# Kernel optimization log

Measured on AMD Instinct MI355X. Metric: run time of the kernel, lower is better.

The kernel has to match this reference:

```python
import jax, jax.numpy as jnp
import numpy as np

B, N, D = 4, 4096, 1024
H, DH = 16, 64
EPS = 1e-5


def setup_inputs() -> dict:
    key = jax.random.key(0)
    ks = jax.random.split(key, 4)
    x = jax.random.normal(ks[0], (B, N, D), dtype=jnp.float32)
    w_qkv = jax.random.normal(ks[1], (D, 3 * H * DH), dtype=jnp.float32) * 0.02
    # per-head LayerNorm affine params (one LayerNorm(dim_head) per head)
    gamma_k = jnp.ones((H, DH), dtype=jnp.float32)
    beta_k = jnp.zeros((H, DH), dtype=jnp.float32)
    gamma_v = jnp.ones((H, DH), dtype=jnp.float32)
    beta_v = jnp.zeros((H, DH), dtype=jnp.float32)
    w_out = jax.random.normal(ks[2], (H * DH, D), dtype=jnp.float32) * 0.02
    b_out = jnp.zeros((D,), dtype=jnp.float32)
    return {"x": x, "w_qkv": w_qkv, "gamma_k": gamma_k, "beta_k": beta_k,
            "gamma_v": gamma_v, "beta_v": beta_v, "w_out": w_out, "b_out": b_out}


def _per_head_layernorm(t, gamma, beta):
    # t: [b, h, n, d]; gamma/beta: [h, d] (distinct affine per head)
    mu = jnp.mean(t, axis=-1, keepdims=True)
    var = jnp.mean(jnp.square(t - mu), axis=-1, keepdims=True)  # biased, as torch LayerNorm
    tn = (t - mu) * jax.lax.rsqrt(var + EPS)
    return tn * gamma[None, :, None, :] + beta[None, :, None, :]


def reference(x, w_qkv, gamma_k, beta_k, gamma_v, beta_v, w_out, b_out):
    b, n, _ = x.shape
    h, dh = gamma_k.shape
    qkv = jnp.einsum('bnd,de->bne', x, w_qkv)  # [b, n, 3*h*dh]
    q, k, v = jnp.split(qkv, 3, axis=-1)

    def to_heads(t):  # b n (h d) -> b h n d
        return t.reshape(b, n, h, dh).transpose(0, 2, 1, 3)

    q, k, v = to_heads(q), to_heads(k), to_heads(v)
    k = _per_head_layernorm(k, gamma_k, beta_k)
    v = _per_head_layernorm(v, gamma_v, beta_v)
    # linear attention: scores = k^T v / n  -> [b, h, d, d]
    scores = jnp.einsum('bhnd,bhne->bhde', k, v) / n
    out = jnp.einsum('bhnd,bhde->bhne', q, scores)  # [b, h, n, d]
    out = out.transpose(0, 2, 1, 3).reshape(b, n, h * dh)
    return jnp.einsum('bne,ed->bnd', out, w_out) + b_out
```

## Files before the change

### kernel.cpp

```cpp
#include <hip/hip_runtime.h>

typedef __attribute__((ext_vector_type(4))) float f32x4;
typedef __attribute__((ext_vector_type(8))) short s16x8;

#define DEV static __device__ __forceinline__

typedef __attribute__((address_space(3))) void lds_t;
typedef __attribute__((address_space(1))) void gbl_t;

DEV void gload_lds16(const void* g, void* l) {
    __builtin_amdgcn_global_load_lds((gbl_t*)g, (lds_t*)l, 16, 0, 0);
}

DEV ushort f2bf(float f) {
    unsigned u = __float_as_uint(f);
    u += 0x7fffu + ((u >> 16) & 1u);
    return (ushort)(u >> 16);
}
DEV float bf2f(ushort h) { return __uint_as_float(((unsigned)h) << 16); }

#define FULLBAR() do {                              \
    __builtin_amdgcn_sched_barrier(0);              \
    asm volatile("" ::: "memory");                  \
    __builtin_amdgcn_s_barrier();                   \
    asm volatile("" ::: "memory");                  \
    __builtin_amdgcn_sched_barrier(0);              \
} while (0)

#define WAITVM(n) asm volatile("s_waitcnt vmcnt(" #n ")" ::: "memory")

__global__ void pack_x_k(const float* __restrict__ x, ushort* __restrict__ xb, int n4) {
    int stride = gridDim.x * blockDim.x;
    for (int i = blockIdx.x * blockDim.x + threadIdx.x; i < n4; i += stride) {
        float4 v = reinterpret_cast<const float4*>(x)[i];
        ushort4 o;
        o.x = f2bf(v.x); o.y = f2bf(v.y); o.z = f2bf(v.z); o.w = f2bf(v.w);
        reinterpret_cast<ushort4*>(xb)[i] = o;
    }
}

__global__ void pack_wq_k(const float* __restrict__ w, ushort* __restrict__ o) {
    int i = blockIdx.x * 256 + threadIdx.x;
    int r = i >> 8, c4 = i & 255;
    float4 v = *reinterpret_cast<const float4*>(w + (size_t)r * 3072 + c4 * 4);
    ushort4 u;
    u.x = f2bf(v.x); u.y = f2bf(v.y); u.z = f2bf(v.z); u.w = f2bf(v.w);
    *reinterpret_cast<ushort4*>(o + (size_t)r * 1024 + c4 * 4) = u;
}

__global__ void trans_pack_k(const float* __restrict__ in, ushort* __restrict__ out,
                             int R, int C, int col0) {
    __shared__ float tile[32][33];
    int bx = col0 + blockIdx.x * 32, by = blockIdx.y * 32;
    int tx = threadIdx.x, ty = threadIdx.y;
#pragma unroll
    for (int i = 0; i < 32; i += 8)
        tile[ty + i][tx] = in[(size_t)(by + ty + i) * C + bx + tx];
    __syncthreads();
#pragma unroll
    for (int i = 0; i < 32; i += 8)
        out[(size_t)(bx - col0 + ty + i) * R + by + tx] = f2bf(tile[tx][ty + i]);
}

template <int MODE>
__global__ __launch_bounds__(512, 2) void gemm_bt_k(
    const ushort* __restrict__ A, const ushort* __restrict__ Bt,
    int Nn, int col0, size_t b_stride,
    ushort* __restrict__ qo, ushort* __restrict__ ko, ushort* __restrict__ vo,
    const float* __restrict__ gk, const float* __restrict__ bk,
    const float* __restrict__ gv, const float* __restrict__ bv,
    const float* __restrict__ bias, float* __restrict__ outf)
{
    __shared__ __align__(16) ushort SH[65536];
    const int t = threadIdx.x;
    const int w = t >> 6, lane = t & 63;
    const int wr = w >> 2, wc = w & 3;
    const int lrow = lane & 15, kh = lane >> 4;

    int bid = blockIdx.y * gridDim.x + blockIdx.x;
    int C8 = (gridDim.x * gridDim.y) >> 3;
    int nid = (bid & 7) * C8 + (bid >> 3);
    int n0 = (nid % gridDim.x) * 256;
    int m0 = (nid / gridDim.x) * 256;

    const ushort* Bte = (MODE == 1) ? Bt + (size_t)(m0 >> 12) * b_stride : Bt;

    const int srow = w * 8 + (lane >> 3);
    const int scol = ((lane & 7) ^ ((lane >> 3) & 7)) * 8;

    f32x4 acc[8][4] = {};

    auto STAGE = [&](int kt, int s) {
        ushort* As = SH + s * 32768;
        ushort* Bs = As + 16384;
        const ushort* Ag = A   + (size_t)(m0 + srow) * 1024 + kt * 64 + scol;
        const ushort* Bg = Bte + (size_t)(n0 + srow) * 1024 + kt * 64 + scol;
#pragma unroll
        for (int c = 0; c < 4; ++c) {
            gload_lds16(Ag + (size_t)(c * 64) * 1024, As + (c * 64 + w * 8) * 64);
            gload_lds16(Bg + (size_t)(c * 64) * 1024, Bs + (c * 64 + w * 8) * 64);
        }
    };

    const int g0 = ((kh) ^ (lrow & 7)) * 8;
    const int g1 = ((4 + kh) ^ (lrow & 7)) * 8;

    auto COMPUTE = [&](int s) {
        const ushort* As = SH + s * 32768;
        const ushort* Bs = As + 16384;
#pragma unroll
        for (int kk = 0; kk < 2; ++kk) {
            const int go = kk ? g1 : g0;
            s16x8 af[8], bfr[4];
#pragma unroll
            for (int mi = 0; mi < 8; mi++)
                af[mi] = *reinterpret_cast<const s16x8*>(&As[(wr * 128 + mi * 16 + lrow) * 64 + go]);
#pragma unroll
            for (int ni = 0; ni < 4; ni++)
                bfr[ni] = *reinterpret_cast<const s16x8*>(&Bs[(wc * 64 + ni * 16 + lrow) * 64 + go]);
            __builtin_amdgcn_s_setprio(1);
#pragma unroll
            for (int mi = 0; mi < 8; mi++)
#pragma unroll
                for (int ni = 0; ni < 4; ni++)
                    acc[mi][ni] = __builtin_amdgcn_mfma_f32_16x16x32_bf16(af[mi], bfr[ni], acc[mi][ni], 0, 0, 0);
            __builtin_amdgcn_s_setprio(0);
        }
    };

    STAGE(0, 0);
    for (int kt = 0; kt < 15; ++kt) {
        STAGE(kt + 1, (kt + 1) & 1);
        WAITVM(8);
        FULLBAR();
        COMPUTE(kt & 1);
        FULLBAR();
    }
    WAITVM(0);
    FULLBAR();
    COMPUTE(1);

    if (MODE == 0) {
        const int e0 = col0 + n0 + wc * 64;
        const int which = e0 >> 10;
        const int h = (e0 >> 6) & 15;
        const float* g  = (which == 1) ? gk : gv;
        const float* bb = (which == 1) ? bk : bv;
        ushort* dst     = (which == 1) ? ko : vo;
        float gr[4], br[4];
#pragma unroll
        for (int ni = 0; ni < 4; ni++) {
            gr[ni] = g[h * 64 + ni * 16 + lrow];
            br[ni] = bb[h * 64 + ni * 16 + lrow];
        }
        __syncthreads();
        ushort* Tl = SH + w * 4608;
#pragma unroll
        for (int chunk = 0; chunk < 2; ++chunk) {
#pragma unroll
            for (int mi2 = 0; mi2 < 4; ++mi2) {
                const int mi = chunk * 4 + mi2;
#pragma unroll
                for (int j = 0; j < 4; j++) {
                    float s = acc[mi][0][j] + acc[mi][1][j] + acc[mi][2][j] + acc[mi][3][j];
                    s += __shfl_xor(s, 1, 64);
                    s += __shfl_xor(s, 2, 64);
                    s += __shfl_xor(s, 4, 64);
                    s += __shfl_xor(s, 8, 64);
                    float mu = s * (1.f / 64.f);
                    float t2 = 0.f;
#pragma unroll
                    for (int ni = 0; ni < 4; ni++) {
                        float dd = acc[mi][ni][j] - mu;
                        t2 += dd * dd;
                    }
                    t2 += __shfl_xor(t2, 1, 64);
                    t2 += __shfl_xor(t2, 2, 64);
                    t2 += __shfl_xor(t2, 4, 64);
                    t2 += __shfl_xor(t2, 8, 64);
                    float inv = rsqrtf(t2 * (1.f / 64.f) + 1e-5f);
#pragma unroll
                    for (int ni = 0; ni < 4; ni++) {
                        float y = (acc[mi][ni][j] - mu) * inv * gr[ni] + br[ni];
                        Tl[(ni * 16 + lrow) * 72 + mi2 * 16 + kh * 4 + j] = f2bf(y);
                    }
                }
            }
            const int mrow0 = m0 + wr * 128 + chunk * 64;
            const int b = mrow0 >> 12, ns0 = mrow0 & 4095;
            ushort* obase = dst + (((size_t)b * 16 + h) * 64) * 4096 + ns0;
#pragma unroll
            for (int p = 0; p < 8; ++p) {
                int d = p * 8 + (lane >> 3);
                int mo = (lane & 7) * 8;
                s16x8 vv = *reinterpret_cast<const s16x8*>(&Tl[d * 72 + mo]);
                *reinterpret_cast<s16x8*>(obase + (size_t)d * 4096 + mo) = vv;
            }
        }
    } else if (MODE == 1) {
#pragma unroll
        for (int mi = 0; mi < 8; mi++)
#pragma unroll
            for (int ni = 0; ni < 4; ni++) {
                int e = n0 + wc * 64 + ni * 16 + lrow;
                float bv2 = bias[e];
#pragma unroll
                for (int j = 0; j < 4; j++) {
                    int m = m0 + wr * 128 + mi * 16 + kh * 4 + j;
                    outf[(size_t)m * Nn + e] = acc[mi][ni][j] + bv2;
                }
            }
    } else {
#pragma unroll
        for (int mi = 0; mi < 8; mi++)
#pragma unroll
            for (int ni = 0; ni < 4; ni++) {
                int e = n0 + wc * 64 + ni * 16 + lrow;
#pragma unroll
                for (int j = 0; j < 4; j++) {
                    int m = m0 + wr * 128 + mi * 16 + kh * 4 + j;
                    qo[(size_t)m * 1024 + e] = f2bf(acc[mi][ni][j]);
                }
            }
    }
}

__global__ __launch_bounds__(256) void scores_k(const ushort* __restrict__ kT,
                                                const ushort* __restrict__ vT,
                                                float* __restrict__ sc)
{
    __shared__ float red[4][64][65];
    const int bh = blockIdx.y;
    const int t = threadIdx.x;
    const int w = t >> 6, lane = t & 63;
    const int lrow = lane & 15, kh = lane >> 4;
    const ushort* ka = kT + (size_t)bh * 64 * 4096;
    const ushort* va = vT + (size_t)bh * 64 * 4096;
    const int n0 = blockIdx.x * 512 + w * 128;

    f32x4 acc[4][4] = {};
#pragma unroll
    for (int ks = 0; ks < 4; ++ks) {
        const int n = n0 + ks * 32 + kh * 8;
        s16x8 af[4], bfr[4];
#pragma unroll
        for (int mi = 0; mi < 4; mi++)
            af[mi] = *reinterpret_cast<const s16x8*>(ka + (size_t)(mi * 16 + lrow) * 4096 + n);
#pragma unroll
        for (int ni = 0; ni < 4; ni++)
            bfr[ni] = *reinterpret_cast<const s16x8*>(va + (size_t)(ni * 16 + lrow) * 4096 + n);
#pragma unroll
        for (int mi = 0; mi < 4; mi++)
#pragma unroll
            for (int ni = 0; ni < 4; ni++)
                acc[mi][ni] = __builtin_amdgcn_mfma_f32_16x16x32_bf16(af[mi], bfr[ni], acc[mi][ni], 0, 0, 0);
    }
#pragma unroll
    for (int mi = 0; mi < 4; mi++)
#pragma unroll
        for (int ni = 0; ni < 4; ni++)
#pragma unroll
            for (int j = 0; j < 4; j++)
                red[w][mi * 16 + kh * 4 + j][ni * 16 + lrow] = acc[mi][ni][j];
    __syncthreads();
    const float scale = 1.f / 4096.f;
    for (int idx = t; idx < 4096; idx += 256) {
        int d = idx >> 6, e = idx & 63;
        float s = red[0][d][e] + red[1][d][e] + red[2][d][e] + red[3][d][e];
        atomicAdd(&sc[(size_t)bh * 4096 + idx], s * scale);
    }
}

__global__ __launch_bounds__(256) void wprime_k(const float* __restrict__ sc,
                                                const ushort* __restrict__ woutT,
                                                ushort* __restrict__ wpT)
{
    __shared__ float scl[64][65];
    __shared__ ushort wl[128][72];
    int bh = blockIdx.y;
    int b = bh >> 4, h = bh & 15;
    int f0 = blockIdx.x * 128;
    int t = threadIdx.x;
    for (int i = t; i < 4096; i += 256) {
        int d2 = i >> 6, e = i & 63;
        scl[e][d2] = sc[(size_t)bh * 4096 + i];
    }
    for (int i = t; i < 1024; i += 256) {
        int fl = i >> 3, c = i & 7;
        *reinterpret_cast<int4*>(&wl[fl][c * 8]) =
            *reinterpret_cast<const int4*>(woutT + (size_t)(f0 + fl) * 1024 + h * 64 + c * 8);
    }
    __syncthreads();
    int dd = (t & 7) * 8;
    int fl0 = t >> 3;
#pragma unroll
    for (int fi = 0; fi < 4; ++fi) {
        int fl = fi * 32 + fl0;
        float acc[8] = {};
        for (int e = 0; e < 64; ++e) {
            float wv = bf2f(wl[fl][e]);
#pragma unroll
            for (int i = 0; i < 8; ++i)
                acc[i] = fmaf(wv, scl[e][dd + i], acc[i]);
        }
        ushort4 o0, o1;
        o0.x = f2bf(acc[0]); o0.y = f2bf(acc[1]); o0.z = f2bf(acc[2]); o0.w = f2bf(acc[3]);
        o1.x = f2bf(acc[4]); o1.y = f2bf(acc[5]); o1.z = f2bf(acc[6]); o1.w = f2bf(acc[7]);
        ushort* op = wpT + ((size_t)b * 1024 + f0 + fl) * 1024 + h * 64 + dd;
        *reinterpret_cast<ushort4*>(op) = o0;
        *reinterpret_cast<ushort4*>(op + 4) = o1;
    }
}

extern "C" void kernel_launch(void* const* d_in, const int* in_sizes, int n_in,
                              void* d_out, int out_size, void* d_ws, size_t ws_size,
                              hipStream_t stream)
{
    const float* x       = (const float*)d_in[0];
    const float* w_qkv   = (const float*)d_in[1];
    const float* gamma_k = (const float*)d_in[2];
    const float* beta_k  = (const float*)d_in[3];
    const float* gamma_v = (const float*)d_in[4];
    const float* beta_v  = (const float*)d_in[5];
    const float* w_out   = (const float*)d_in[6];
    const float* b_out   = (const float*)d_in[7];
    float* out = (float*)d_out;

    char* ws = (char*)d_ws;
    const size_t MB = 1024 * 1024;
    ushort* xb    = (ushort*)(ws);
    ushort* wkvT  = (ushort*)(ws + 32 * MB);
    ushort* woutT = (ushort*)(ws + 38 * MB);
    ushort* wqb   = (ushort*)(ws + 40 * MB);
    ushort* kb    = (ushort*)(ws + 48 * MB);
    ushort* vb    = (ushort*)(ws + 80 * MB);
    float*  sc    = (float*)(ws + 112 * MB);
    ushort* wpT   = (ushort*)(ws + 120 * MB);
    ushort* fT    = (ushort*)(ws + 128 * MB);

    pack_x_k<<<2048, 256, 0, stream>>>(x, xb, 16384 * 1024 / 4);
    pack_wq_k<<<1024, 256, 0, stream>>>(w_qkv, wqb);
    trans_pack_k<<<dim3(64, 32), dim3(32, 8), 0, stream>>>(w_qkv, wkvT, 1024, 3072, 1024);
    trans_pack_k<<<dim3(32, 32), dim3(32, 8), 0, stream>>>(w_out, woutT, 1024, 1024, 0);
    gemm_bt_k<0><<<dim3(8, 64), 512, 0, stream>>>(xb, wkvT, 2048, 1024, 0,
                                                  nullptr, kb, vb,
                                                  gamma_k, beta_k, gamma_v, beta_v,
                                                  nullptr, nullptr);
    hipMemsetAsync(sc, 0, 64 * 4096 * sizeof(float), stream);
    scores_k<<<dim3(8, 64), 256, 0, stream>>>(kb, vb, sc);
    wprime_k<<<dim3(8, 64), 256, 0, stream>>>(sc, woutT, wpT);
    gemm_bt_k<2><<<dim3(4, 16), 512, 0, stream>>>(wpT, wqb, 1024, 0, 0,
                                                  fT, nullptr, nullptr,
                                                  nullptr, nullptr, nullptr, nullptr,
                                                  nullptr, nullptr);
    gemm_bt_k<1><<<dim3(4, 64), 512, 0, stream>>>(xb, fT, 1024, 0, (size_t)1048576,
                                                  nullptr, nullptr, nullptr,
                                                  nullptr, nullptr, nullptr, nullptr,
                                                  b_out, out);
}
```

Measured before the change: 225.6 us.

## Split GEMM main loop into four interleaved sub-phases with staggered A/B prefetch

Restructures the bf16 MFMA GEMM main loop so each K tile is processed in four sub-phases of two M-fragments each. Global-to-LDS loads for the next A tile and the tile after next for B are issued between phases, and B fragments are loaded once per tile and held in registers. The aim is to overlap LDS reads, global loads and MFMA work more finely, in the style of a ping-pong schedule. It adds many more barriers per tile and depends on the vmcnt accounting staying correct.

```diff
diff --git a/kernel.cpp b/kernel.cpp
--- a/kernel.cpp
+++ b/kernel.cpp
@@ -28,6 +28,10 @@
 } while (0)
 
 #define WAITVM(n) asm volatile("s_waitcnt vmcnt(" #n ")" ::: "memory")
+#define LGKM0() do {                                        \
+    asm volatile("s_waitcnt lgkmcnt(0)" ::: "memory");      \
+    __builtin_amdgcn_sched_barrier(0);                      \
+} while (0)
 
 __global__ void pack_x_k(const float* __restrict__ x, ushort* __restrict__ xb, int n4) {
     int stride = gridDim.x * blockDim.x;
@@ -85,60 +89,92 @@
 
     const ushort* Bte = (MODE == 1) ? Bt + (size_t)(m0 >> 12) * b_stride : Bt;
 
-    const int srow = w * 8 + (lane >> 3);
+    const int srow8 = w * 8 + (lane >> 3);
     const int scol = ((lane & 7) ^ ((lane >> 3) & 7)) * 8;
 
+    const int g0 = ((kh) ^ (lrow & 7)) * 8;
+    const int g1 = ((4 + kh) ^ (lrow & 7)) * 8;
+
     f32x4 acc[8][4] = {};
-
-    auto STAGE = [&](int kt, int s) {
+    s16x8 bfr[4][2];
+
+    auto STAGE_A = [&](int kt, int s, int h) {
         ushort* As = SH + s * 32768;
-        ushort* Bs = As + 16384;
-        const ushort* Ag = A   + (size_t)(m0 + srow) * 1024 + kt * 64 + scol;
-        const ushort* Bg = Bte + (size_t)(n0 + srow) * 1024 + kt * 64 + scol;
-#pragma unroll
-        for (int c = 0; c < 4; ++c) {
-            gload_lds16(Ag + (size_t)(c * 64) * 1024, As + (c * 64 + w * 8) * 64);
-            gload_lds16(Bg + (size_t)(c * 64) * 1024, Bs + (c * 64 + w * 8) * 64);
+        const ushort* Ag = A + (size_t)(m0 + h * 128 + srow8) * 1024 + kt * 64 + scol;
+        gload_lds16(Ag,                     As + (h * 128 + w * 8) * 64);
+        gload_lds16(Ag + (size_t)64 * 1024, As + (h * 128 + 64 + w * 8) * 64);
+    };
+    auto STAGE_B = [&](int kt, int s, int h) {
+        ushort* Bs = SH + s * 32768 + 16384;
+        const ushort* Bg = Bte + (size_t)(n0 + h * 128 + srow8) * 1024 + kt * 64 + scol;
+        gload_lds16(Bg,                     Bs + (h * 128 + w * 8) * 64);
+        gload_lds16(Bg + (size_t)64 * 1024, Bs + (h * 128 + 64 + w * 8) * 64);
+    };
+    auto DS_B = [&](int s) {
+        const ushort* Bs = SH + s * 32768 + 16384;
+#pragma unroll
+        for (int ni = 0; ni < 4; ni++) {
+            const int r = (wc * 64 + ni * 16 + lrow) * 64;
+            bfr[ni][0] = *reinterpret_cast<const s16x8*>(&Bs[r + g0]);
+            bfr[ni][1] = *reinterpret_cast<const s16x8*>(&Bs[r + g1]);
         }
     };
 
-    const int g0 = ((kh) ^ (lrow & 7)) * 8;
-    const int g1 = ((4 + kh) ^ (lrow & 7)) * 8;
-
-    auto COMPUTE = [&](int s) {
-        const ushort* As = SH + s * 32768;
-        const ushort* Bs = As + 16384;
-#pragma unroll
-        for (int kk = 0; kk < 2; ++kk) {
-            const int go = kk ? g1 : g0;
-            s16x8 af[8], bfr[4];
-#pragma unroll
-            for (int mi = 0; mi < 8; mi++)
-                af[mi] = *reinterpret_cast<const s16x8*>(&As[(wr * 128 + mi * 16 + lrow) * 64 + go]);
-#pragma unroll
-            for (int ni = 0; ni < 4; ni++)
-                bfr[ni] = *reinterpret_cast<const s16x8*>(&Bs[(wc * 64 + ni * 16 + lrow) * 64 + go]);
-            __builtin_amdgcn_s_setprio(1);
-#pragma unroll
-            for (int mi = 0; mi < 8; mi++)
-#pragma unroll
-                for (int ni = 0; ni < 4; ni++)
-                    acc[mi][ni] = __builtin_amdgcn_mfma_f32_16x16x32_bf16(af[mi], bfr[ni], acc[mi][ni], 0, 0, 0);
-            __builtin_amdgcn_s_setprio(0);
-        }
-    };
-
-    STAGE(0, 0);
-    for (int kt = 0; kt < 15; ++kt) {
-        STAGE(kt + 1, (kt + 1) & 1);
-        WAITVM(8);
+#define DSA(MI0)                                                              \
+    _Pragma("unroll")                                                         \
+    for (int i = 0; i < 2; i++) {                                             \
+        const int r = (wr * 128 + ((MI0) + i) * 16 + lrow) * 64;              \
+        af[i][0] = *reinterpret_cast<const s16x8*>(&As[r + g0]);              \
+        af[i][1] = *reinterpret_cast<const s16x8*>(&As[r + g1]);              \
+    }
+
+#define MFMA16(MI0)                                                           \
+    __builtin_amdgcn_s_setprio(1);                                            \
+    _Pragma("unroll")                                                         \
+    for (int kk = 0; kk < 2; kk++)                                            \
+        _Pragma("unroll")                                                     \
+        for (int i = 0; i < 2; i++)                                           \
+            _Pragma("unroll")                                                 \
+            for (int ni = 0; ni < 4; ni++)                                    \
+                acc[(MI0) + i][ni] = __builtin_amdgcn_mfma_f32_16x16x32_bf16( \
+                    af[i][kk], bfr[ni][kk], acc[(MI0) + i][ni], 0, 0, 0);     \
+    __builtin_amdgcn_s_setprio(0);
+
+    STAGE_A(0, 0, 0); STAGE_A(0, 0, 1);
+    STAGE_B(0, 0, 0); STAGE_B(0, 0, 1);
+    STAGE_B(1, 1, 0); STAGE_B(1, 1, 1);
+    WAITVM(4);
+    FULLBAR();
+
+    for (int kt = 0; kt < 16; ++kt) {
+        const int p = kt & 1, q = p ^ 1;
+        const ushort* As = SH + p * 32768;
+        s16x8 af[2][2];
+        DS_B(p);
+        DSA(0);
+        if (kt + 1 < 16) STAGE_A(kt + 1, q, 0);
+        FULLBAR(); LGKM0();
+        MFMA16(0);
         FULLBAR();
-        COMPUTE(kt & 1);
+        DSA(2);
+        if (kt + 1 < 16) STAGE_A(kt + 1, q, 1);
+        FULLBAR(); LGKM0();
+        MFMA16(2);
         FULLBAR();
-    }
-    WAITVM(0);
-    FULLBAR();
-    COMPUTE(1);
+        DSA(4);
+        if (kt + 2 < 16) STAGE_B(kt + 2, p, 0);
+        FULLBAR(); LGKM0();
+        MFMA16(4);
+        FULLBAR();
+        DSA(6);
+        if (kt + 2 < 16) STAGE_B(kt + 2, p, 1);
+        if (kt < 14) { WAITVM(4); } else { WAITVM(0); }
+        FULLBAR(); LGKM0();
+        MFMA16(6);
+        FULLBAR();
+    }
+#undef DSA
+#undef MFMA16
 
     if (MODE == 0) {
         const int e0 = col0 + n0 + wc * 64;
@@ -190,8 +226,8 @@
             const int b = mrow0 >> 12, ns0 = mrow0 & 4095;
             ushort* obase = dst + (((size_t)b * 16 + h) * 64) * 4096 + ns0;
 #pragma unroll
-            for (int p = 0; p < 8; ++p) {
-                int d = p * 8 + (lane >> 3);
+            for (int p2 = 0; p2 < 8; ++p2) {
+                int d = p2 * 8 + (lane >> 3);
                 int mo = (lane & 7) * 8;
                 s16x8 vv = *reinterpret_cast<const s16x8*>(&Tl[d * 72 + mo]);
                 *reinterpret_cast<s16x8*>(obase + (size_t)d * 4096 + mo) = vv;
```

New measurement: 223.8 us. About the same (-0.8%).

## Restage GEMM pipeline with split A/B prefetch and add dedicated fold GEMM kernel

Applied to the files above, without the earlier changes.

The main bf16 GEMM loop is restructured: B tiles are prefetched two k-steps ahead and A tiles one step ahead, and each k-step is split into two half-k MFMA phases. Loads are issued between the phases, so the second barrier per iteration sits in the middle of the compute instead of at the end. Launch bounds change from 2 to 1 blocks per CU, allowing more registers per thread, since B fragments for both halves are now held. The small weight-folding GEMM (MODE 2, a 4x16 grid of 256x256 tiles) is replaced by a separate 128x128-tile kernel with a 3-stage pipeline, launched as 256 blocks to fill more CUs.

```diff
diff --git a/kernel.cpp b/kernel.cpp
--- a/kernel.cpp
+++ b/kernel.cpp
@@ -28,6 +28,7 @@
 } while (0)
 
 #define WAITVM(n) asm volatile("s_waitcnt vmcnt(" #n ")" ::: "memory")
+#define LGKM0() asm volatile("s_waitcnt lgkmcnt(0)" ::: "memory")
 
 __global__ void pack_x_k(const float* __restrict__ x, ushort* __restrict__ xb, int n4) {
     int stride = gridDim.x * blockDim.x;
@@ -63,10 +64,10 @@
 }
 
 template <int MODE>
-__global__ __launch_bounds__(512, 2) void gemm_bt_k(
+__global__ __launch_bounds__(512, 1) void gemm_bt_k(
     const ushort* __restrict__ A, const ushort* __restrict__ Bt,
     int Nn, int col0, size_t b_stride,
-    ushort* __restrict__ qo, ushort* __restrict__ ko, ushort* __restrict__ vo,
+    ushort* __restrict__ ko, ushort* __restrict__ vo,
     const float* __restrict__ gk, const float* __restrict__ bk,
     const float* __restrict__ gv, const float* __restrict__ bv,
     const float* __restrict__ bias, float* __restrict__ outf)
@@ -85,60 +86,76 @@
 
     const ushort* Bte = (MODE == 1) ? Bt + (size_t)(m0 >> 12) * b_stride : Bt;
 
-    const int srow = w * 8 + (lane >> 3);
+    const int srow8 = w * 8 + (lane >> 3);
     const int scol = ((lane & 7) ^ ((lane >> 3) & 7)) * 8;
-
-    f32x4 acc[8][4] = {};
-
-    auto STAGE = [&](int kt, int s) {
-        ushort* As = SH + s * 32768;
-        ushort* Bs = As + 16384;
-        const ushort* Ag = A   + (size_t)(m0 + srow) * 1024 + kt * 64 + scol;
-        const ushort* Bg = Bte + (size_t)(n0 + srow) * 1024 + kt * 64 + scol;
-#pragma unroll
-        for (int c = 0; c < 4; ++c) {
-            gload_lds16(Ag + (size_t)(c * 64) * 1024, As + (c * 64 + w * 8) * 64);
-            gload_lds16(Bg + (size_t)(c * 64) * 1024, Bs + (c * 64 + w * 8) * 64);
-        }
-    };
 
     const int g0 = ((kh) ^ (lrow & 7)) * 8;
     const int g1 = ((4 + kh) ^ (lrow & 7)) * 8;
 
-    auto COMPUTE = [&](int s) {
-        const ushort* As = SH + s * 32768;
+    f32x4 acc[8][4] = {};
+    s16x8 bfr[4][2];
+    s16x8 af[8];
+
+    auto STAGE_A = [&](int kt, int s, int h) {
+        ushort* As = SH + s * 32768;
+        const ushort* Ag = A + (size_t)(m0 + h * 128 + srow8) * 1024 + kt * 64 + scol;
+        gload_lds16(Ag,                     As + (h * 128 + w * 8) * 64);
+        gload_lds16(Ag + (size_t)64 * 1024, As + (h * 128 + 64 + w * 8) * 64);
+    };
+    auto STAGE_B = [&](int kt, int s, int h) {
+        ushort* Bs = SH + s * 32768 + 16384;
+        const ushort* Bg = Bte + (size_t)(n0 + h * 128 + srow8) * 1024 + kt * 64 + scol;
+        gload_lds16(Bg,                     Bs + (h * 128 + w * 8) * 64);
+        gload_lds16(Bg + (size_t)64 * 1024, Bs + (h * 128 + 64 + w * 8) * 64);
+    };
+
+    STAGE_A(0, 0, 0); STAGE_A(0, 0, 1);
+    STAGE_B(0, 0, 0); STAGE_B(0, 0, 1);
+    STAGE_B(1, 1, 0); STAGE_B(1, 1, 1);
+
+    for (int kt = 0; kt < 16; ++kt) {
+        const int p = kt & 1, q = p ^ 1;
+        const ushort* As = SH + p * 32768;
         const ushort* Bs = As + 16384;
-#pragma unroll
-        for (int kk = 0; kk < 2; ++kk) {
-            const int go = kk ? g1 : g0;
-            s16x8 af[8], bfr[4];
-#pragma unroll
-            for (int mi = 0; mi < 8; mi++)
-                af[mi] = *reinterpret_cast<const s16x8*>(&As[(wr * 128 + mi * 16 + lrow) * 64 + go]);
+
+        if (kt < 15) { WAITVM(4); } else { WAITVM(0); }
+        FULLBAR();
+
+#pragma unroll
+        for (int ni = 0; ni < 4; ni++) {
+            const int r = (wc * 64 + ni * 16 + lrow) * 64;
+            bfr[ni][0] = *reinterpret_cast<const s16x8*>(&Bs[r + g0]);
+            bfr[ni][1] = *reinterpret_cast<const s16x8*>(&Bs[r + g1]);
+        }
+#pragma unroll
+        for (int mi = 0; mi < 8; mi++)
+            af[mi] = *reinterpret_cast<const s16x8*>(&As[(wr * 128 + mi * 16 + lrow) * 64 + g0]);
+        if (kt + 1 < 16) { STAGE_A(kt + 1, q, 0); STAGE_A(kt + 1, q, 1); }
+
+        __builtin_amdgcn_s_setprio(1);
+#pragma unroll
+        for (int mi = 0; mi < 8; mi++)
 #pragma unroll
             for (int ni = 0; ni < 4; ni++)
-                bfr[ni] = *reinterpret_cast<const s16x8*>(&Bs[(wc * 64 + ni * 16 + lrow) * 64 + go]);
-            __builtin_amdgcn_s_setprio(1);
-#pragma unroll
-            for (int mi = 0; mi < 8; mi++)
-#pragma unroll
-                for (int ni = 0; ni < 4; ni++)
-                    acc[mi][ni] = __builtin_amdgcn_mfma_f32_16x16x32_bf16(af[mi], bfr[ni], acc[mi][ni], 0, 0, 0);
-            __builtin_amdgcn_s_setprio(0);
-        }
-    };
-
-    STAGE(0, 0);
-    for (int kt = 0; kt < 15; ++kt) {
-        STAGE(kt + 1, (kt + 1) & 1);
-        WAITVM(8);
+                acc[mi][ni] = __builtin_amdgcn_mfma_f32_16x16x32_bf16(af[mi], bfr[ni][0], acc[mi][ni], 0, 0, 0);
+        __builtin_amdgcn_s_setprio(0);
+
+        LGKM0();
         FULLBAR();
-        COMPUTE(kt & 1);
-        FULLBAR();
-    }
-    WAITVM(0);
-    FULLBAR();
-    COMPUTE(1);
+
+        if (kt + 2 < 16) { STAGE_B(kt + 2, p, 0); STAGE_B(kt + 2, p, 1); }
+#pragma unroll
+        for (int mi = 0; mi < 8; mi++)
+            af[mi] = *reinterpret_cast<const s16x8*>(&As[(wr * 128 + mi * 16 + lrow) * 64 + g1]);
+
+        __builtin_amdgcn_s_setprio(1);
+#pragma unroll
+        for (int mi = 0; mi < 8; mi++)
+#pragma unroll
+            for (int ni = 0; ni < 4; ni++)
+                acc[mi][ni] = __builtin_amdgcn_mfma_f32_16x16x32_bf16(af[mi], bfr[ni][1], acc[mi][ni], 0, 0, 0);
+        __builtin_amdgcn_s_setprio(0);
+    }
 
     if (MODE == 0) {
         const int e0 = col0 + n0 + wc * 64;
@@ -190,14 +207,14 @@
             const int b = mrow0 >> 12, ns0 = mrow0 & 4095;
             ushort* obase = dst + (((size_t)b * 16 + h) * 64) * 4096 + ns0;
 #pragma unroll
-            for (int p = 0; p < 8; ++p) {
-                int d = p * 8 + (lane >> 3);
+            for (int p2 = 0; p2 < 8; ++p2) {
+                int d = p2 * 8 + (lane >> 3);
                 int mo = (lane & 7) * 8;
                 s16x8 vv = *reinterpret_cast<const s16x8*>(&Tl[d * 72 + mo]);
                 *reinterpret_cast<s16x8*>(obase + (size_t)d * 4096 + mo) = vv;
             }
         }
-    } else if (MODE == 1) {
+    } else {
 #pragma unroll
         for (int mi = 0; mi < 8; mi++)
 #pragma unroll
@@ -210,19 +227,81 @@
                     outf[(size_t)m * Nn + e] = acc[mi][ni][j] + bv2;
                 }
             }
-    } else {
-#pragma unroll
-        for (int mi = 0; mi < 8; mi++)
-#pragma unroll
-            for (int ni = 0; ni < 4; ni++) {
-                int e = n0 + wc * 64 + ni * 16 + lrow;
-#pragma unroll
-                for (int j = 0; j < 4; j++) {
-                    int m = m0 + wr * 128 + mi * 16 + kh * 4 + j;
-                    qo[(size_t)m * 1024 + e] = f2bf(acc[mi][ni][j]);
-                }
+    }
+}
+
+__global__ __launch_bounds__(256) void fold_k(const ushort* __restrict__ A,
+                                              const ushort* __restrict__ Bt,
+                                              ushort* __restrict__ out)
+{
+    __shared__ __align__(16) ushort SH2[24576];
+    const int t = threadIdx.x;
+    const int w = t >> 6, lane = t & 63;
+    const int wm = w >> 1, wn = w & 1;
+    const int lrow = lane & 15, kh = lane >> 4;
+    const int n0 = blockIdx.x * 128, m0 = blockIdx.y * 128;
+
+    const int srow0 = w * 32 + (lane >> 2);
+    const int scolSwz = (((lane & 3) ^ ((lane >> 3) & 3)) * 8);
+
+    f32x4 acc[4][4] = {};
+
+    auto STAGE = [&](int kt, int s) {
+        ushort* As = SH2 + s * 8192;
+        ushort* Bs = As + 4096;
+        const ushort* Ag = A  + (size_t)(m0 + srow0) * 1024 + kt * 32 + scolSwz;
+        const ushort* Bg = Bt + (size_t)(n0 + srow0) * 1024 + kt * 32 + scolSwz;
+        gload_lds16(Ag,             As + w * 1024);
+        gload_lds16(Bg,             Bs + w * 1024);
+        gload_lds16(Ag + 16 * 1024, As + w * 1024 + 512);
+        gload_lds16(Bg + 16 * 1024, Bs + w * 1024 + 512);
+    };
+
+    const int rdoff = (kh ^ ((lrow >> 1) & 3)) * 8;
+
+    auto COMPUTE = [&](int s) {
+        const ushort* As = SH2 + s * 8192;
+        const ushort* Bs = As + 4096;
+        s16x8 af[4], bfr[4];
+#pragma unroll
+        for (int mi = 0; mi < 4; mi++)
+            af[mi] = *reinterpret_cast<const s16x8*>(&As[(wm * 64 + mi * 16 + lrow) * 32 + rdoff]);
+#pragma unroll
+        for (int ni = 0; ni < 4; ni++)
+            bfr[ni] = *reinterpret_cast<const s16x8*>(&Bs[(wn * 64 + ni * 16 + lrow) * 32 + rdoff]);
+#pragma unroll
+        for (int mi = 0; mi < 4; mi++)
+#pragma unroll
+            for (int ni = 0; ni < 4; ni++)
+                acc[mi][ni] = __builtin_amdgcn_mfma_f32_16x16x32_bf16(af[mi], bfr[ni], acc[mi][ni], 0, 0, 0);
+    };
+
+    STAGE(0, 0);
+    STAGE(1, 1);
+    int ss = 2, sc_ = 0;
+    for (int kt = 0; kt < 30; ++kt) {
+        STAGE(kt + 2, ss);
+        ss = (ss == 2) ? 0 : ss + 1;
+        WAITVM(8);
+        FULLBAR();
+        COMPUTE(sc_);
+        sc_ = (sc_ == 2) ? 0 : sc_ + 1;
+        FULLBAR();
+    }
+    WAITVM(4); FULLBAR(); COMPUTE(0); FULLBAR();
+    WAITVM(0); FULLBAR(); COMPUTE(1);
+
+#pragma unroll
+    for (int mi = 0; mi < 4; mi++)
+#pragma unroll
+        for (int ni = 0; ni < 4; ni++) {
+            int e = n0 + wn * 64 + ni * 16 + lrow;
+#pragma unroll
+            for (int j = 0; j < 4; j++) {
+                int m = m0 + wm * 64 + mi * 16 + kh * 4 + j;
+                out[(size_t)m * 1024 + e] = f2bf(acc[mi][ni][j]);
             }
-    }
+        }
 }
 
 __global__ __launch_bounds__(256) void scores_k(const ushort* __restrict__ kT,
@@ -343,18 +422,15 @@
     trans_pack_k<<<dim3(64, 32), dim3(32, 8), 0, stream>>>(w_qkv, wkvT, 1024, 3072, 1024);
     trans_pack_k<<<dim3(32, 32), dim3(32, 8), 0, stream>>>(w_out, woutT, 1024, 1024, 0);
     gemm_bt_k<0><<<dim3(8, 64), 512, 0, stream>>>(xb, wkvT, 2048, 1024, 0,
-                                                  nullptr, kb, vb,
+                                                  kb, vb,
                                                   gamma_k, beta_k, gamma_v, beta_v,
                                                   nullptr, nullptr);
     hipMemsetAsync(sc, 0, 64 * 4096 * sizeof(float), stream);
     scores_k<<<dim3(8, 64), 256, 0, stream>>>(kb, vb, sc);
     wprime_k<<<dim3(8, 64), 256, 0, stream>>>(sc, woutT, wpT);
-    gemm_bt_k<2><<<dim3(4, 16), 512, 0, stream>>>(wpT, wqb, 1024, 0, 0,
-                                                  fT, nullptr, nullptr,
-                                                  nullptr, nullptr, nullptr, nullptr,
-                                                  nullptr, nullptr);
+    fold_k<<<dim3(8, 32), 256, 0, stream>>>(wpT, wqb, fT);
     gemm_bt_k<1><<<dim3(4, 64), 512, 0, stream>>>(xb, fT, 1024, 0, (size_t)1048576,
-                                                  nullptr, nullptr, nullptr,
+                                                  nullptr, nullptr,
                                                   nullptr, nullptr, nullptr, nullptr,
                                                   b_out, out);
 }
```

Result: faster. 213.9 us (-5.2%).
